# Kernel optimization log

Measured on AMD Instinct MI355X. Metric: run time of the kernel, lower is better.

The kernel has to match this reference:

```python
import jax, jax.numpy as jnp
import numpy as np

N_NODES = 50000
N_EDGES = 1250000
IN_CH, HID_CH, OUT_CH = 128, 64, 10
N_GRAPHS = 500


def gcn_conv(x, W, src, dst, n_nodes):
    # GCNConv (bias=False, normalize=True, add_self_loops=True):
    # out = D^{-1/2} (A + I) D^{-1/2} X W
    h = x @ W  # [N, H]
    loop = jnp.arange(n_nodes, dtype=src.dtype)
    s = jnp.concatenate([src, loop])
    d = jnp.concatenate([dst, loop])
    deg = jax.ops.segment_sum(jnp.ones_like(d, dtype=h.dtype), d, num_segments=n_nodes)
    dinv = jnp.where(deg > 0, jax.lax.rsqrt(deg), 0.0)
    norm = dinv[s] * dinv[d]  # [E+N]
    msgs = h[s] * norm[:, None]  # gather + normalize
    return jax.ops.segment_sum(msgs, d, num_segments=n_nodes)  # scatter-add


def setup_inputs() -> dict:
    key = jax.random.key(0)
    ks = jax.random.split(key, 8)
    x = jax.random.normal(ks[0], (N_NODES, IN_CH), dtype=jnp.float32)
    edge_index = jax.random.randint(ks[1], (2, N_EDGES), 0, N_NODES, dtype=jnp.int64)
    batch = jnp.sort(jax.random.randint(ks[2], (N_NODES,), 0, N_GRAPHS, dtype=jnp.int64))
    def glorot(k, fan_in, fan_out):
        lim = np.sqrt(6.0 / (fan_in + fan_out))
        return jax.random.uniform(k, (fan_in, fan_out), jnp.float32, -lim, lim)
    W1 = glorot(ks[3], IN_CH, HID_CH)
    W2 = glorot(ks[4], HID_CH, HID_CH)
    W3 = glorot(ks[5], HID_CH, HID_CH)
    Wl = glorot(ks[6], HID_CH, OUT_CH)
    bl = jnp.zeros((OUT_CH,), jnp.float32)
    return {"x": x, "edge_index": edge_index, "batch": batch,
            "W1": W1, "W2": W2, "W3": W3, "Wl": Wl, "bl": bl}


def reference(x, edge_index, batch, W1, W2, W3, Wl, bl):
    src, dst = edge_index[0], edge_index[1]
    n = x.shape[0]
    h = jax.nn.relu(gcn_conv(x, W1, src, dst, n))
    h = jax.nn.relu(gcn_conv(h, W2, src, dst, n))
    h = gcn_conv(h, W3, src, dst, n)
    # global_mean_pool over graph ids
    sums = jax.ops.segment_sum(h, batch, num_segments=N_GRAPHS)
    cnts = jax.ops.segment_sum(jnp.ones((n,), h.dtype), batch, num_segments=N_GRAPHS)
    pooled = sums / jnp.maximum(cnts, 1.0)[:, None]
    return pooled @ Wl + bl
```

## Files before the change

kernel.cpp:

```cpp
#include <hip/hip_runtime.h>

#define CH 64
#define CHUNK 4096
#define BSHIFT 8
#define NBUCK 196

__device__ __forceinline__ unsigned short f2bf_rne(float f) {
    unsigned int u = __float_as_uint(f);
    u += 0x7fffu + ((u >> 16) & 1u);
    return (unsigned short)(u >> 16);
}
__device__ __forceinline__ float bf_lo(unsigned int q) {
    return __uint_as_float(q << 16);
}
__device__ __forceinline__ float bf_hi(unsigned int q) {
    return __uint_as_float(q & 0xffff0000u);
}
__device__ __forceinline__ unsigned int pack2bf(float lo, float hi) {
    return (unsigned int)f2bf_rne(lo) | ((unsigned int)f2bf_rne(hi) << 16);
}

__global__ __launch_bounds__(256) void bucket_hist_kernel(
        const int* __restrict__ dst, int* __restrict__ bucket_cnt, int E) {
    __shared__ int hist[256];
    int tid = threadIdx.x;
    int e0 = blockIdx.x * CHUNK;
    int total = min(CHUNK, E - e0);
    hist[tid] = 0;
    __syncthreads();
    for (int i = tid; i < total; i += 256)
        atomicAdd(&hist[dst[e0 + i] >> BSHIFT], 1);
    __syncthreads();
    if (tid < NBUCK && hist[tid]) atomicAdd(&bucket_cnt[tid], hist[tid]);
}

__global__ __launch_bounds__(256) void bucket_scan_kernel(
        const int* __restrict__ cnt, int* __restrict__ base,
        int* __restrict__ cursor, int* __restrict__ rowptr, int N, int E) {
    __shared__ int sc[256];
    int tid = threadIdx.x;
    int c = (tid < NBUCK) ? cnt[tid] : 0;
    sc[tid] = c;
    __syncthreads();
    for (int off = 1; off < 256; off <<= 1) {
        int v = (tid >= off) ? sc[tid - off] : 0;
        __syncthreads();
        sc[tid] += v;
        __syncthreads();
    }
    if (tid < NBUCK) { base[tid] = sc[tid] - c; cursor[tid] = sc[tid] - c; }
    if (tid == NBUCK - 1) base[NBUCK] = sc[tid];
    if (tid == 0) rowptr[N] = E;
}

__global__ __launch_bounds__(256) void bin_kernel(
        const int* __restrict__ src, const int* __restrict__ dst,
        int* __restrict__ cursor, unsigned int* __restrict__ pairs, int E) {
    __shared__ unsigned int stage[CHUNK];
    __shared__ int hist[256], sc[256], lbase[256], lcur[256], gbase[256];
    int tid = threadIdx.x;
    int e0 = blockIdx.x * CHUNK;
    int total = min(CHUNK, E - e0);
    hist[tid] = 0;
    __syncthreads();
    for (int i = tid; i < total; i += 256)
        atomicAdd(&hist[dst[e0 + i] >> BSHIFT], 1);
    __syncthreads();
    sc[tid] = hist[tid];
    __syncthreads();
    for (int off = 1; off < 256; off <<= 1) {
        int v = (tid >= off) ? sc[tid - off] : 0;
        __syncthreads();
        sc[tid] += v;
        __syncthreads();
    }
    lbase[tid] = sc[tid] - hist[tid];
    lcur[tid]  = sc[tid] - hist[tid];
    if (tid < NBUCK && hist[tid] > 0) gbase[tid] = atomicAdd(&cursor[tid], hist[tid]);
    __syncthreads();
    for (int i = tid; i < total; i += 256) {
        unsigned int s = (unsigned int)src[e0 + i];
        unsigned int d = (unsigned int)dst[e0 + i];
        int pos = atomicAdd(&lcur[d >> BSHIFT], 1);
        stage[pos] = (d << 16) | s;
    }
    __syncthreads();
    for (int i = tid; i < total; i += 256) {
        unsigned int p = stage[i];
        int b = (int)(p >> 24);
        pairs[gbase[b] + (i - lbase[b])] = p;
    }
}

__global__ __launch_bounds__(256) void bucket_sort_kernel(
        const unsigned int* __restrict__ pairs, const int* __restrict__ base,
        int* __restrict__ csr, int* __restrict__ rowptr,
        float* __restrict__ dinv, int N) {
    __shared__ int cntl[256], sc[256], cur[256];
    int tid = threadIdx.x;
    int b = blockIdx.x;
    int pbase = base[b], pend = base[b + 1];
    int cnt = pend - pbase;
    cntl[tid] = 0;
    __syncthreads();
    for (int i = tid; i < cnt; i += 256)
        atomicAdd(&cntl[(pairs[pbase + i] >> 16) & 255u], 1);
    __syncthreads();
    sc[tid] = cntl[tid];
    __syncthreads();
    for (int off = 1; off < 256; off <<= 1) {
        int v = (tid >= off) ? sc[tid - off] : 0;
        __syncthreads();
        sc[tid] += v;
        __syncthreads();
    }
    int excl = sc[tid] - cntl[tid];
    cur[tid] = excl;
    int v = (b << BSHIFT) + tid;
    if (v < N) {
        rowptr[v] = pbase + excl;
        dinv[v] = rsqrtf((float)(cntl[tid] + 1));
    }
    __syncthreads();
    for (int i = tid; i < cnt; i += 256) {
        unsigned int p = pairs[pbase + i];
        int pos = atomicAdd(&cur[(p >> 16) & 255u], 1);
        csr[pbase + pos] = (int)(p & 0xffffu);
    }
}

template <int K>
__global__ __launch_bounds__(256) void gemm_f32_kernel(
        const float* __restrict__ X, const float* __restrict__ W,
        const float* __restrict__ dinv, unsigned short* __restrict__ G, int N) {
    constexpr int KC  = 64;
    constexpr int XLD = KC + 4;
    __shared__ float Xs[64 * XLD];
    __shared__ float Wls[KC * CH];
    int tid = threadIdx.x;
    int tx  = tid & 15;
    int ty  = tid >> 4;
    int row_tile = blockIdx.x * 64;
    int r0 = ty * 4;
    float acc[4][4] = {{0.f}};

    for (int kc = 0; kc < K; kc += KC) {
        __syncthreads();
#pragma unroll
        for (int t = 0; t < 4; ++t) {
            int idx = tid + t * 256;
            int row = idx >> 4;
            int k4  = idx & 15;
            int grow = row_tile + row;
            const float4* xs = (const float4*)(X + (size_t)min(grow, N - 1) * K + kc);
            *(float4*)&Xs[row * XLD + 4 * k4] = xs[k4];
        }
#pragma unroll
        for (int t = 0; t < 4; ++t) {
            int idx = tid + t * 256;
            *(float4*)&Wls[idx * 4] = ((const float4*)(W + (size_t)kc * CH))[idx];
        }
        __syncthreads();
#pragma unroll
        for (int kk = 0; kk < KC; kk += 4) {
            float xr[4][4], wr[4][4];
#pragma unroll
            for (int i = 0; i < 4; ++i) {
                float4 v = *(const float4*)&Xs[(r0 + i) * XLD + kk];
                xr[i][0] = v.x; xr[i][1] = v.y; xr[i][2] = v.z; xr[i][3] = v.w;
            }
#pragma unroll
            for (int j = 0; j < 4; ++j) {
                float4 v = *(const float4*)&Wls[(kk + j) * CH + 4 * tx];
                wr[j][0] = v.x; wr[j][1] = v.y; wr[j][2] = v.z; wr[j][3] = v.w;
            }
#pragma unroll
            for (int i = 0; i < 4; ++i)
#pragma unroll
                for (int j = 0; j < 4; ++j)
#pragma unroll
                    for (int c = 0; c < 4; ++c)
                        acc[i][c] = fmaf(xr[i][j], wr[j][c], acc[i][c]);
        }
    }
#pragma unroll
    for (int i = 0; i < 4; ++i) {
        int r = row_tile + r0 + i;
        if (r < N) {
            float d = dinv[r];
            ushort4 o;
            o.x = f2bf_rne(acc[i][0] * d);
            o.y = f2bf_rne(acc[i][1] * d);
            o.z = f2bf_rne(acc[i][2] * d);
            o.w = f2bf_rne(acc[i][3] * d);
            ((ushort4*)G)[(size_t)r * 16 + tx] = o;
        }
    }
}

__global__ __launch_bounds__(256) void gemm_bf16_kernel(
        const unsigned short* __restrict__ Xbf, const float* __restrict__ W,
        const float* __restrict__ dinv, unsigned short* __restrict__ G, int N) {
    constexpr int XLDU = 36;
    __shared__ unsigned int Xs[64 * XLDU];
    __shared__ float Wls[64 * CH];
    int tid = threadIdx.x;
    int tx  = tid & 15;
    int ty  = tid >> 4;
    int row_tile = blockIdx.x * 64;
    int r0 = ty * 4;
    float acc[4][4] = {{0.f}};

#pragma unroll
    for (int t = 0; t < 2; ++t) {
        int idx = tid + t * 256;
        int row = idx >> 3;
        int k4  = idx & 7;
        int grow = row_tile + row;
        uint4 v = ((const uint4*)Xbf)[(size_t)min(grow, N - 1) * 8 + k4];
        *(uint4*)&Xs[row * XLDU + 4 * k4] = v;
    }
#pragma unroll
    for (int t = 0; t < 4; ++t) {
        int idx = tid + t * 256;
        *(float4*)&Wls[idx * 4] = ((const float4*)W)[idx];
    }
    __syncthreads();
#pragma unroll
    for (int kk = 0; kk < 64; kk += 4) {
        float xr[4][4], wr[4][4];
#pragma unroll
        for (int i = 0; i < 4; ++i) {
            uint2 q = *(const uint2*)&Xs[(r0 + i) * XLDU + (kk >> 1)];
            xr[i][0] = bf_lo(q.x); xr[i][1] = bf_hi(q.x);
            xr[i][2] = bf_lo(q.y); xr[i][3] = bf_hi(q.y);
        }
#pragma unroll
        for (int j = 0; j < 4; ++j) {
            float4 v = *(const float4*)&Wls[(kk + j) * CH + 4 * tx];
            wr[j][0] = v.x; wr[j][1] = v.y; wr[j][2] = v.z; wr[j][3] = v.w;
        }
#pragma unroll
        for (int i = 0; i < 4; ++i)
#pragma unroll
            for (int j = 0; j < 4; ++j)
#pragma unroll
                for (int c = 0; c < 4; ++c)
                    acc[i][c] = fmaf(xr[i][j], wr[j][c], acc[i][c]);
    }
#pragma unroll
    for (int i = 0; i < 4; ++i) {
        int r = row_tile + r0 + i;
        if (r < N) {
            float d = dinv[r];
            ushort4 o;
            o.x = f2bf_rne(acc[i][0] * d);
            o.y = f2bf_rne(acc[i][1] * d);
            o.z = f2bf_rne(acc[i][2] * d);
            o.w = f2bf_rne(acc[i][3] * d);
            ((ushort4*)G)[(size_t)r * 16 + tx] = o;
        }
    }
}

template <bool F32OUT>
__global__ __launch_bounds__(256) void aggregate_kernel(
        const unsigned short* __restrict__ G, const int* __restrict__ rowptr,
        const int* __restrict__ csr, const float* __restrict__ dinv,
        void* __restrict__ Out, int N, int E, int relu) {
    int lane = threadIdx.x & 63;
    int w = (blockIdx.x * 256 + threadIdx.x) >> 6;
    int grp = lane >> 3;
    int cl  = lane & 7;
    int v = w * 8 + grp;
    bool valid = v < N;
    int vc = valid ? v : N - 1;
    int beg = rowptr[vc];
    int cnt = valid ? rowptr[vc + 1] - beg : 0;
    int mx = cnt;
    mx = max(mx, __shfl_xor(mx, 8));
    mx = max(mx, __shfl_xor(mx, 16));
    mx = max(mx, __shfl_xor(mx, 32));

    const uint4* __restrict__ G4 = (const uint4*)G;
    float a0 = 0.f, a1 = 0.f, a2 = 0.f, a3 = 0.f;
    float a4 = 0.f, a5 = 0.f, a6 = 0.f, a7 = 0.f;
#pragma unroll 2
    for (int it = 0; it < mx; ++it) {
        int eg = min(beg + it, E - 1);
        bool ok = it < cnt;
        int u = ok ? csr[eg] : 0;
        float s = ok ? 1.f : 0.f;
        uint4 q = G4[(size_t)u * 8 + cl];
        a0 = fmaf(bf_lo(q.x), s, a0); a1 = fmaf(bf_hi(q.x), s, a1);
        a2 = fmaf(bf_lo(q.y), s, a2); a3 = fmaf(bf_hi(q.y), s, a3);
        a4 = fmaf(bf_lo(q.z), s, a4); a5 = fmaf(bf_hi(q.z), s, a5);
        a6 = fmaf(bf_lo(q.w), s, a6); a7 = fmaf(bf_hi(q.w), s, a7);
    }
    if (valid) {
        uint4 q = G4[(size_t)v * 8 + cl];
        float d = dinv[v];
        float o0 = (a0 + bf_lo(q.x)) * d, o1 = (a1 + bf_hi(q.x)) * d;
        float o2 = (a2 + bf_lo(q.y)) * d, o3 = (a3 + bf_hi(q.y)) * d;
        float o4 = (a4 + bf_lo(q.z)) * d, o5 = (a5 + bf_hi(q.z)) * d;
        float o6 = (a6 + bf_lo(q.w)) * d, o7 = (a7 + bf_hi(q.w)) * d;
        if (relu) {
            o0 = fmaxf(o0, 0.f); o1 = fmaxf(o1, 0.f); o2 = fmaxf(o2, 0.f);
            o3 = fmaxf(o3, 0.f); o4 = fmaxf(o4, 0.f); o5 = fmaxf(o5, 0.f);
            o6 = fmaxf(o6, 0.f); o7 = fmaxf(o7, 0.f);
        }
        if (F32OUT) {
            float4 w0 = {o0, o1, o2, o3}, w1 = {o4, o5, o6, o7};
            ((float4*)Out)[(size_t)v * 16 + cl * 2]     = w0;
            ((float4*)Out)[(size_t)v * 16 + cl * 2 + 1] = w1;
        } else {
            uint4 p;
            p.x = pack2bf(o0, o1); p.y = pack2bf(o2, o3);
            p.z = pack2bf(o4, o5); p.w = pack2bf(o6, o7);
            ((uint4*)Out)[(size_t)v * 8 + cl] = p;
        }
    }
}

__global__ void gptr_kernel(const int* __restrict__ batch, int* __restrict__ gptr,
                            int N, int NG) {
    int g = blockIdx.x * blockDim.x + threadIdx.x;
    if (g > NG) return;
    if (g == NG) { gptr[NG] = N; return; }
    int lo = 0, hi = N;
    while (lo < hi) {
        int mid = (lo + hi) >> 1;
        if (batch[mid] < g) lo = mid + 1; else hi = mid;
    }
    gptr[g] = lo;
}

__global__ __launch_bounds__(64) void pool_head_kernel(
        const float* __restrict__ H, const int* __restrict__ gptr,
        const float* __restrict__ Wl, const float* __restrict__ bl,
        float* __restrict__ out, int NG) {
    int g = blockIdx.x;
    int lane = threadIdx.x;
    int s = gptr[g], e = gptr[g + 1];
    float acc = 0.f;
    for (int v = s; v < e; ++v) acc += H[(size_t)v * CH + lane];
    float c = (float)(e - s);
    float mean = (c > 0.f) ? acc / c : 0.f;
    for (int o = 0; o < 10; ++o) {
        float t = mean * Wl[lane * 10 + o];
        for (int off = 32; off > 0; off >>= 1) t += __shfl_down(t, off);
        if (lane == 0) out[g * 10 + o] = t + bl[o];
    }
}

extern "C" void kernel_launch(void* const* d_in, const int* in_sizes, int n_in,
                              void* d_out, int out_size, void* d_ws, size_t ws_size,
                              hipStream_t stream) {
    const float* x     = (const float*)d_in[0];
    const int*   ei    = (const int*)d_in[1];
    const int*   batch = (const int*)d_in[2];
    const float* W1    = (const float*)d_in[3];
    const float* W2    = (const float*)d_in[4];
    const float* W3    = (const float*)d_in[5];
    const float* Wl    = (const float*)d_in[6];
    const float* bl    = (const float*)d_in[7];
    float* out = (float*)d_out;

    const int N  = in_sizes[0] / 128;
    const int E  = in_sizes[1] / 2;
    const int NG = out_size / 10;

    const int* src = ei;
    const int* dst = ei + E;

    char* ws = (char*)d_ws;
    size_t off = 0;
    auto alloc = [&](size_t bytes) -> void* {
        void* p = ws + off;
        off += bytes;
        off = (off + 255) & ~(size_t)255;
        return p;
    };
    int*   bucket_cnt    = (int*)alloc((size_t)NBUCK * 4);
    int*   bucket_base   = (int*)alloc((size_t)(NBUCK + 1) * 4);
    int*   bucket_cursor = (int*)alloc((size_t)NBUCK * 4);
    int*   csr    = (int*)alloc((size_t)(E + 64) * 4);
    int*   rowptr = (int*)alloc((size_t)(N + 1) * 4);
    float* dinv   = (float*)alloc((size_t)N * 4);
    int*   gptr   = (int*)alloc((size_t)(NG + 1) * 4);
    unsigned short* Gbf = (unsigned short*)alloc((size_t)N * CH * 2);
    unsigned short* Hbf = (unsigned short*)alloc((size_t)N * CH * 2);
    float* hbuf   = (float*)alloc((size_t)N * CH * 4);
    unsigned int* pairs = (unsigned int*)hbuf;

    hipMemsetAsync(bucket_cnt, 0, (size_t)NBUCK * 4, stream);

    int cb = (E + CHUNK - 1) / CHUNK;
    int ab = ((N + 7) / 8 + 3) / 4;
    int gb = (N + 63) / 64;

    bucket_hist_kernel<<<cb, 256, 0, stream>>>(dst, bucket_cnt, E);
    bucket_scan_kernel<<<1, 256, 0, stream>>>(bucket_cnt, bucket_base, bucket_cursor,
                                              rowptr, N, E);
    bin_kernel<<<cb, 256, 0, stream>>>(src, dst, bucket_cursor, pairs, E);
    bucket_sort_kernel<<<NBUCK, 256, 0, stream>>>(pairs, bucket_base, csr, rowptr, dinv, N);
    gptr_kernel<<<(NG + 512) / 512, 512, 0, stream>>>(batch, gptr, N, NG);

    gemm_f32_kernel<128><<<gb, 256, 0, stream>>>(x, W1, dinv, Gbf, N);
    aggregate_kernel<false><<<ab, 256, 0, stream>>>(Gbf, rowptr, csr, dinv, Hbf, N, E, 1);
    gemm_bf16_kernel<<<gb, 256, 0, stream>>>(Hbf, W2, dinv, Gbf, N);
    aggregate_kernel<false><<<ab, 256, 0, stream>>>(Gbf, rowptr, csr, dinv, Hbf, N, E, 1);
    gemm_bf16_kernel<<<gb, 256, 0, stream>>>(Hbf, W3, dinv, Gbf, N);
    aggregate_kernel<true><<<ab, 256, 0, stream>>>(Gbf, rowptr, csr, dinv, hbuf, N, E, 0);

    pool_head_kernel<<<NG, 64, 0, stream>>>(hbuf, gptr, Wl, bl, out, NG);
}
```

Measured before the change: 251.2 us.

## Fuse first GEMM with edge histogram, use per-chunk offsets and 16-bit CSR

Runs the first GEMM and the per-chunk destination histogram as one launch, so the GEMM no longer waits for dinv. The first aggregation therefore applies the source dinv per edge. A single scan kernel computes deterministic per-chunk bucket offsets, replacing the memset, the global atomic cursor and the separate scan. Graph pointers are computed inside that same scan kernel, and CSR column indices are stored as 16-bit values to halve index traffic. The costs are an extra per-edge dinv gather in layer one and a serial loop over chunks in a single scan block.

```diff
diff --git a/kernel.cpp b/kernel.cpp
--- a/kernel.cpp
+++ b/kernel.cpp
@@ -20,42 +20,138 @@
     return (unsigned int)f2bf_rne(lo) | ((unsigned int)f2bf_rne(hi) << 16);
 }
 
-__global__ __launch_bounds__(256) void bucket_hist_kernel(
-        const int* __restrict__ dst, int* __restrict__ bucket_cnt, int E) {
+template <int K>
+__global__ __launch_bounds__(256) void gemm1_hist_kernel(
+        const float* __restrict__ X, const float* __restrict__ W,
+        unsigned short* __restrict__ G, int N,
+        const int* __restrict__ dst, int* __restrict__ chunk_hist, int E,
+        int gemm_blocks) {
+    constexpr int KC  = 64;
+    constexpr int XLD = KC + 4;
+    __shared__ float Xs[64 * XLD];
+    __shared__ float Wls[KC * CH];
     __shared__ int hist[256];
     int tid = threadIdx.x;
-    int e0 = blockIdx.x * CHUNK;
-    int total = min(CHUNK, E - e0);
-    hist[tid] = 0;
-    __syncthreads();
-    for (int i = tid; i < total; i += 256)
-        atomicAdd(&hist[dst[e0 + i] >> BSHIFT], 1);
-    __syncthreads();
-    if (tid < NBUCK && hist[tid]) atomicAdd(&bucket_cnt[tid], hist[tid]);
-}
-
-__global__ __launch_bounds__(256) void bucket_scan_kernel(
-        const int* __restrict__ cnt, int* __restrict__ base,
-        int* __restrict__ cursor, int* __restrict__ rowptr, int N, int E) {
-    __shared__ int sc[256];
-    int tid = threadIdx.x;
-    int c = (tid < NBUCK) ? cnt[tid] : 0;
-    sc[tid] = c;
-    __syncthreads();
-    for (int off = 1; off < 256; off <<= 1) {
-        int v = (tid >= off) ? sc[tid - off] : 0;
-        __syncthreads();
-        sc[tid] += v;
-        __syncthreads();
-    }
-    if (tid < NBUCK) { base[tid] = sc[tid] - c; cursor[tid] = sc[tid] - c; }
-    if (tid == NBUCK - 1) base[NBUCK] = sc[tid];
-    if (tid == 0) rowptr[N] = E;
+
+    if (blockIdx.x >= gemm_blocks) {
+        int cid = blockIdx.x - gemm_blocks;
+        int e0 = cid * CHUNK;
+        int total = min(CHUNK, E - e0);
+        hist[tid] = 0;
+        __syncthreads();
+        for (int i = tid; i < total; i += 256)
+            atomicAdd(&hist[dst[e0 + i] >> BSHIFT], 1);
+        __syncthreads();
+        if (tid < NBUCK) chunk_hist[cid * NBUCK + tid] = hist[tid];
+        return;
+    }
+
+    int tx  = tid & 15;
+    int ty  = tid >> 4;
+    int row_tile = blockIdx.x * 64;
+    int r0 = ty * 4;
+    float acc[4][4] = {{0.f}};
+
+    for (int kc = 0; kc < K; kc += KC) {
+        __syncthreads();
+#pragma unroll
+        for (int t = 0; t < 4; ++t) {
+            int idx = tid + t * 256;
+            int row = idx >> 4;
+            int k4  = idx & 15;
+            int grow = row_tile + row;
+            const float4* xs = (const float4*)(X + (size_t)min(grow, N - 1) * K + kc);
+            *(float4*)&Xs[row * XLD + 4 * k4] = xs[k4];
+        }
+#pragma unroll
+        for (int t = 0; t < 4; ++t) {
+            int idx = tid + t * 256;
+            *(float4*)&Wls[idx * 4] = ((const float4*)(W + (size_t)kc * CH))[idx];
+        }
+        __syncthreads();
+#pragma unroll
+        for (int kk = 0; kk < KC; kk += 4) {
+            float xr[4][4], wr[4][4];
+#pragma unroll
+            for (int i = 0; i < 4; ++i) {
+                float4 v = *(const float4*)&Xs[(r0 + i) * XLD + kk];
+                xr[i][0] = v.x; xr[i][1] = v.y; xr[i][2] = v.z; xr[i][3] = v.w;
+            }
+#pragma unroll
+            for (int j = 0; j < 4; ++j) {
+                float4 v = *(const float4*)&Wls[(kk + j) * CH + 4 * tx];
+                wr[j][0] = v.x; wr[j][1] = v.y; wr[j][2] = v.z; wr[j][3] = v.w;
+            }
+#pragma unroll
+            for (int i = 0; i < 4; ++i)
+#pragma unroll
+                for (int j = 0; j < 4; ++j)
+#pragma unroll
+                    for (int c = 0; c < 4; ++c)
+                        acc[i][c] = fmaf(xr[i][j], wr[j][c], acc[i][c]);
+        }
+    }
+#pragma unroll
+    for (int i = 0; i < 4; ++i) {
+        int r = row_tile + r0 + i;
+        if (r < N) {
+            ushort4 o;
+            o.x = f2bf_rne(acc[i][0]);
+            o.y = f2bf_rne(acc[i][1]);
+            o.z = f2bf_rne(acc[i][2]);
+            o.w = f2bf_rne(acc[i][3]);
+            ((ushort4*)G)[(size_t)r * 16 + tx] = o;
+        }
+    }
+}
+
+__global__ __launch_bounds__(256) void scan_gptr_kernel(
+        const int* __restrict__ chunk_hist, int cb,
+        int* __restrict__ chunk_base, int* __restrict__ bucket_base,
+        int* __restrict__ rowptr,
+        const int* __restrict__ batch, int* __restrict__ gptr,
+        int N, int E, int NG) {
+    if (blockIdx.x == 0) {
+        __shared__ int sc[256];
+        int t = threadIdx.x;
+        int total = 0;
+        if (t < NBUCK)
+            for (int c = 0; c < cb; ++c) total += chunk_hist[c * NBUCK + t];
+        sc[t] = total;
+        __syncthreads();
+        for (int off = 1; off < 256; off <<= 1) {
+            int v = (t >= off) ? sc[t - off] : 0;
+            __syncthreads();
+            sc[t] += v;
+            __syncthreads();
+        }
+        int base = sc[t] - total;
+        if (t < NBUCK) {
+            bucket_base[t] = base;
+            int run = base;
+            for (int c = 0; c < cb; ++c) {
+                chunk_base[c * NBUCK + t] = run;
+                run += chunk_hist[c * NBUCK + t];
+            }
+        }
+        if (t == NBUCK - 1) bucket_base[NBUCK] = sc[t];
+        if (t == 0) rowptr[N] = E;
+    } else {
+        for (int g = threadIdx.x; g <= NG; g += 256) {
+            if (g == NG) { gptr[NG] = N; continue; }
+            int lo = 0, hi = N;
+            while (lo < hi) {
+                int mid = (lo + hi) >> 1;
+                if (batch[mid] < g) lo = mid + 1; else hi = mid;
+            }
+            gptr[g] = lo;
+        }
+    }
 }
 
 __global__ __launch_bounds__(256) void bin_kernel(
         const int* __restrict__ src, const int* __restrict__ dst,
-        int* __restrict__ cursor, unsigned int* __restrict__ pairs, int E) {
+        const int* __restrict__ chunk_base, unsigned int* __restrict__ pairs, int E) {
     __shared__ unsigned int stage[CHUNK];
     __shared__ int hist[256], sc[256], lbase[256], lcur[256], gbase[256];
     int tid = threadIdx.x;
@@ -76,7 +172,7 @@
     }
     lbase[tid] = sc[tid] - hist[tid];
     lcur[tid]  = sc[tid] - hist[tid];
-    if (tid < NBUCK && hist[tid] > 0) gbase[tid] = atomicAdd(&cursor[tid], hist[tid]);
+    if (tid < NBUCK) gbase[tid] = chunk_base[blockIdx.x * NBUCK + tid];
     __syncthreads();
     for (int i = tid; i < total; i += 256) {
         unsigned int s = (unsigned int)src[e0 + i];
@@ -94,7 +190,7 @@
 
 __global__ __launch_bounds__(256) void bucket_sort_kernel(
         const unsigned int* __restrict__ pairs, const int* __restrict__ base,
-        int* __restrict__ csr, int* __restrict__ rowptr,
+        unsigned short* __restrict__ csr, int* __restrict__ rowptr,
         float* __restrict__ dinv, int N) {
     __shared__ int cntl[256], sc[256], cur[256];
     int tid = threadIdx.x;
@@ -125,75 +221,67 @@
     for (int i = tid; i < cnt; i += 256) {
         unsigned int p = pairs[pbase + i];
         int pos = atomicAdd(&cur[(p >> 16) & 255u], 1);
-        csr[pbase + pos] = (int)(p & 0xffffu);
-    }
-}
-
-template <int K>
-__global__ __launch_bounds__(256) void gemm_f32_kernel(
-        const float* __restrict__ X, const float* __restrict__ W,
-        const float* __restrict__ dinv, unsigned short* __restrict__ G, int N) {
-    constexpr int KC  = 64;
-    constexpr int XLD = KC + 4;
-    __shared__ float Xs[64 * XLD];
-    __shared__ float Wls[KC * CH];
-    int tid = threadIdx.x;
-    int tx  = tid & 15;
-    int ty  = tid >> 4;
-    int row_tile = blockIdx.x * 64;
-    int r0 = ty * 4;
-    float acc[4][4] = {{0.f}};
-
-    for (int kc = 0; kc < K; kc += KC) {
-        __syncthreads();
-#pragma unroll
-        for (int t = 0; t < 4; ++t) {
-            int idx = tid + t * 256;
-            int row = idx >> 4;
-            int k4  = idx & 15;
-            int grow = row_tile + row;
-            const float4* xs = (const float4*)(X + (size_t)min(grow, N - 1) * K + kc);
-            *(float4*)&Xs[row * XLD + 4 * k4] = xs[k4];
-        }
-#pragma unroll
-        for (int t = 0; t < 4; ++t) {
-            int idx = tid + t * 256;
-            *(float4*)&Wls[idx * 4] = ((const float4*)(W + (size_t)kc * CH))[idx];
-        }
-        __syncthreads();
-#pragma unroll
-        for (int kk = 0; kk < KC; kk += 4) {
-            float xr[4][4], wr[4][4];
-#pragma unroll
-            for (int i = 0; i < 4; ++i) {
-                float4 v = *(const float4*)&Xs[(r0 + i) * XLD + kk];
-                xr[i][0] = v.x; xr[i][1] = v.y; xr[i][2] = v.z; xr[i][3] = v.w;
-            }
-#pragma unroll
-            for (int j = 0; j < 4; ++j) {
-                float4 v = *(const float4*)&Wls[(kk + j) * CH + 4 * tx];
-                wr[j][0] = v.x; wr[j][1] = v.y; wr[j][2] = v.z; wr[j][3] = v.w;
-            }
-#pragma unroll
-            for (int i = 0; i < 4; ++i)
-#pragma unroll
-                for (int j = 0; j < 4; ++j)
-#pragma unroll
-                    for (int c = 0; c < 4; ++c)
-                        acc[i][c] = fmaf(xr[i][j], wr[j][c], acc[i][c]);
-        }
-    }
-#pragma unroll
-    for (int i = 0; i < 4; ++i) {
-        int r = row_tile + r0 + i;
-        if (r < N) {
-            float d = dinv[r];
-            ushort4 o;
-            o.x = f2bf_rne(acc[i][0] * d);
-            o.y = f2bf_rne(acc[i][1] * d);
-            o.z = f2bf_rne(acc[i][2] * d);
-            o.w = f2bf_rne(acc[i][3] * d);
-            ((ushort4*)G)[(size_t)r * 16 + tx] = o;
+        csr[pbase + pos] = (unsigned short)(p & 0xffffu);
+    }
+}
+
+template <bool PRESCALED, bool F32OUT>
+__global__ __launch_bounds__(256) void aggregate_kernel(
+        const unsigned short* __restrict__ G, const int* __restrict__ rowptr,
+        const unsigned short* __restrict__ csr, const float* __restrict__ dinv,
+        void* __restrict__ Out, int N, int E, int relu) {
+    int lane = threadIdx.x & 63;
+    int w = (blockIdx.x * 256 + threadIdx.x) >> 6;
+    int grp = lane >> 3, cl = lane & 7;
+    int v = w * 8 + grp;
+    bool valid = v < N;
+    int vc = valid ? v : N - 1;
+    int beg = rowptr[vc];
+    int cnt = valid ? rowptr[vc + 1] - beg : 0;
+    int mx = cnt;
+    mx = max(mx, __shfl_xor(mx, 8));
+    mx = max(mx, __shfl_xor(mx, 16));
+    mx = max(mx, __shfl_xor(mx, 32));
+
+    const uint4* __restrict__ G4 = (const uint4*)G;
+    float a0 = 0.f, a1 = 0.f, a2 = 0.f, a3 = 0.f;
+    float a4 = 0.f, a5 = 0.f, a6 = 0.f, a7 = 0.f;
+#pragma unroll 2
+    for (int it = 0; it < mx; ++it) {
+        int eg = min(beg + it, E - 1);
+        bool ok = it < cnt;
+        int u = ok ? (int)csr[eg] : 0;
+        float s;
+        if (PRESCALED) s = ok ? 1.f : 0.f;
+        else           s = ok ? dinv[u] : 0.f;
+        uint4 q = G4[(size_t)u * 8 + cl];
+        a0 = fmaf(bf_lo(q.x), s, a0); a1 = fmaf(bf_hi(q.x), s, a1);
+        a2 = fmaf(bf_lo(q.y), s, a2); a3 = fmaf(bf_hi(q.y), s, a3);
+        a4 = fmaf(bf_lo(q.z), s, a4); a5 = fmaf(bf_hi(q.z), s, a5);
+        a6 = fmaf(bf_lo(q.w), s, a6); a7 = fmaf(bf_hi(q.w), s, a7);
+    }
+    if (valid) {
+        uint4 q = G4[(size_t)v * 8 + cl];
+        float d = dinv[v];
+        float sv = PRESCALED ? 1.f : d;
+        float o0 = (a0 + bf_lo(q.x) * sv) * d, o1 = (a1 + bf_hi(q.x) * sv) * d;
+        float o2 = (a2 + bf_lo(q.y) * sv) * d, o3 = (a3 + bf_hi(q.y) * sv) * d;
+        float o4 = (a4 + bf_lo(q.z) * sv) * d, o5 = (a5 + bf_hi(q.z) * sv) * d;
+        float o6 = (a6 + bf_lo(q.w) * sv) * d, o7 = (a7 + bf_hi(q.w) * sv) * d;
+        if (relu) {
+            o0 = fmaxf(o0, 0.f); o1 = fmaxf(o1, 0.f); o2 = fmaxf(o2, 0.f);
+            o3 = fmaxf(o3, 0.f); o4 = fmaxf(o4, 0.f); o5 = fmaxf(o5, 0.f);
+            o6 = fmaxf(o6, 0.f); o7 = fmaxf(o7, 0.f);
+        }
+        if (F32OUT) {
+            float4 w0 = {o0, o1, o2, o3}, w1 = {o4, o5, o6, o7};
+            ((float4*)Out)[(size_t)v * 16 + cl * 2]     = w0;
+            ((float4*)Out)[(size_t)v * 16 + cl * 2 + 1] = w1;
+        } else {
+            uint4 p;
+            p.x = pack2bf(o0, o1); p.y = pack2bf(o2, o3);
+            p.z = pack2bf(o4, o5); p.w = pack2bf(o6, o7);
+            ((uint4*)Out)[(size_t)v * 8 + cl] = p;
         }
     }
 }
@@ -261,78 +349,6 @@
             ((ushort4*)G)[(size_t)r * 16 + tx] = o;
         }
     }
-}
-
-template <bool F32OUT>
-__global__ __launch_bounds__(256) void aggregate_kernel(
-        const unsigned short* __restrict__ G, const int* __restrict__ rowptr,
-        const int* __restrict__ csr, const float* __restrict__ dinv,
-        void* __restrict__ Out, int N, int E, int relu) {
-    int lane = threadIdx.x & 63;
-    int w = (blockIdx.x * 256 + threadIdx.x) >> 6;
-    int grp = lane >> 3;
-    int cl  = lane & 7;
-    int v = w * 8 + grp;
-    bool valid = v < N;
-    int vc = valid ? v : N - 1;
-    int beg = rowptr[vc];
-    int cnt = valid ? rowptr[vc + 1] - beg : 0;
-    int mx = cnt;
-    mx = max(mx, __shfl_xor(mx, 8));
-    mx = max(mx, __shfl_xor(mx, 16));
-    mx = max(mx, __shfl_xor(mx, 32));
-
-    const uint4* __restrict__ G4 = (const uint4*)G;
-    float a0 = 0.f, a1 = 0.f, a2 = 0.f, a3 = 0.f;
-    float a4 = 0.f, a5 = 0.f, a6 = 0.f, a7 = 0.f;
-#pragma unroll 2
-    for (int it = 0; it < mx; ++it) {
-        int eg = min(beg + it, E - 1);
-        bool ok = it < cnt;
-        int u = ok ? csr[eg] : 0;
-        float s = ok ? 1.f : 0.f;
-        uint4 q = G4[(size_t)u * 8 + cl];
-        a0 = fmaf(bf_lo(q.x), s, a0); a1 = fmaf(bf_hi(q.x), s, a1);
-        a2 = fmaf(bf_lo(q.y), s, a2); a3 = fmaf(bf_hi(q.y), s, a3);
-        a4 = fmaf(bf_lo(q.z), s, a4); a5 = fmaf(bf_hi(q.z), s, a5);
-        a6 = fmaf(bf_lo(q.w), s, a6); a7 = fmaf(bf_hi(q.w), s, a7);
-    }
-    if (valid) {
-        uint4 q = G4[(size_t)v * 8 + cl];
-        float d = dinv[v];
-        float o0 = (a0 + bf_lo(q.x)) * d, o1 = (a1 + bf_hi(q.x)) * d;
-        float o2 = (a2 + bf_lo(q.y)) * d, o3 = (a3 + bf_hi(q.y)) * d;
-        float o4 = (a4 + bf_lo(q.z)) * d, o5 = (a5 + bf_hi(q.z)) * d;
-        float o6 = (a6 + bf_lo(q.w)) * d, o7 = (a7 + bf_hi(q.w)) * d;
-        if (relu) {
-            o0 = fmaxf(o0, 0.f); o1 = fmaxf(o1, 0.f); o2 = fmaxf(o2, 0.f);
-            o3 = fmaxf(o3, 0.f); o4 = fmaxf(o4, 0.f); o5 = fmaxf(o5, 0.f);
-            o6 = fmaxf(o6, 0.f); o7 = fmaxf(o7, 0.f);
-        }
-        if (F32OUT) {
-            float4 w0 = {o0, o1, o2, o3}, w1 = {o4, o5, o6, o7};
-            ((float4*)Out)[(size_t)v * 16 + cl * 2]     = w0;
-            ((float4*)Out)[(size_t)v * 16 + cl * 2 + 1] = w1;
-        } else {
-            uint4 p;
-            p.x = pack2bf(o0, o1); p.y = pack2bf(o2, o3);
-            p.z = pack2bf(o4, o5); p.w = pack2bf(o6, o7);
-            ((uint4*)Out)[(size_t)v * 8 + cl] = p;
-        }
-    }
-}
-
-__global__ void gptr_kernel(const int* __restrict__ batch, int* __restrict__ gptr,
-                            int N, int NG) {
-    int g = blockIdx.x * blockDim.x + threadIdx.x;
-    if (g > NG) return;
-    if (g == NG) { gptr[NG] = N; return; }
-    int lo = 0, hi = N;
-    while (lo < hi) {
-        int mid = (lo + hi) >> 1;
-        if (batch[mid] < g) lo = mid + 1; else hi = mid;
-    }
-    gptr[g] = lo;
 }
 
 __global__ __launch_bounds__(64) void pool_head_kernel(
@@ -373,6 +389,8 @@
     const int* src = ei;
     const int* dst = ei + E;
 
+    const int cb = (E + CHUNK - 1) / CHUNK;
+
     char* ws = (char*)d_ws;
     size_t off = 0;
     auto alloc = [&](size_t bytes) -> void* {
@@ -381,37 +399,36 @@
         off = (off + 255) & ~(size_t)255;
         return p;
     };
-    int*   bucket_cnt    = (int*)alloc((size_t)NBUCK * 4);
-    int*   bucket_base   = (int*)alloc((size_t)(NBUCK + 1) * 4);
-    int*   bucket_cursor = (int*)alloc((size_t)NBUCK * 4);
-    int*   csr    = (int*)alloc((size_t)(E + 64) * 4);
+    int*   chunk_hist  = (int*)alloc((size_t)cb * NBUCK * 4);
+    int*   chunk_base  = (int*)alloc((size_t)cb * NBUCK * 4);
+    int*   bucket_base = (int*)alloc((size_t)(NBUCK + 1) * 4);
+    unsigned short* csr = (unsigned short*)alloc((size_t)(E + 64) * 2);
     int*   rowptr = (int*)alloc((size_t)(N + 1) * 4);
     float* dinv   = (float*)alloc((size_t)N * 4);
-    int*   gptr   = (int*)alloc((size_t)(NG + 1) * 4);
-    unsigned short* Gbf = (unsigned short*)alloc((size_t)N * CH * 2);
-    unsigned short* Hbf = (unsigned short*)alloc((size_t)N * CH * 2);
+    int*   gptrb  = (int*)alloc((size_t)(NG + 1) * 4);
+    unsigned short* GA = (unsigned short*)alloc((size_t)N * CH * 2);
+    unsigned short* GB = (unsigned short*)alloc((size_t)N * CH * 2);
     float* hbuf   = (float*)alloc((size_t)N * CH * 4);
     unsigned int* pairs = (unsigned int*)hbuf;
 
-    hipMemsetAsync(bucket_cnt, 0, (size_t)NBUCK * 4, stream);
-
-    int cb = (E + CHUNK - 1) / CHUNK;
+    int gb = (N + 63) / 64;
     int ab = ((N + 7) / 8 + 3) / 4;
-    int gb = (N + 63) / 64;
-
-    bucket_hist_kernel<<<cb, 256, 0, stream>>>(dst, bucket_cnt, E);
-    bucket_scan_kernel<<<1, 256, 0, stream>>>(bucket_cnt, bucket_base, bucket_cursor,
-                                              rowptr, N, E);
-    bin_kernel<<<cb, 256, 0, stream>>>(src, dst, bucket_cursor, pairs, E);
+
+    gemm1_hist_kernel<128><<<gb + cb, 256, 0, stream>>>(x, W1, GA, N,
+                                                        dst, chunk_hist, E, gb);
+    scan_gptr_kernel<<<2, 256, 0, stream>>>(chunk_hist, cb, chunk_base, bucket_base,
+                                            rowptr, batch, gptrb, N, E, NG);
+    bin_kernel<<<cb, 256, 0, stream>>>(src, dst, chunk_base, pairs, E);
     bucket_sort_kernel<<<NBUCK, 256, 0, stream>>>(pairs, bucket_base, csr, rowptr, dinv, N);
-    gptr_kernel<<<(NG + 512) / 512, 512, 0, stream>>>(batch, gptr, N, NG);
-
-    gemm_f32_kernel<128><<<gb, 256, 0, stream>>>(x, W1, dinv, Gbf, N);
-    aggregate_kernel<false><<<ab, 256, 0, stream>>>(Gbf, rowptr, csr, dinv, Hbf, N, E, 1);
-    gemm_bf16_kernel<<<gb, 256, 0, stream>>>(Hbf, W2, dinv, Gbf, N);
-    aggregate_kernel<false><<<ab, 256, 0, stream>>>(Gbf, rowptr, csr, dinv, Hbf, N, E, 1);
-    gemm_bf16_kernel<<<gb, 256, 0, stream>>>(Hbf, W3, dinv, Gbf, N);
-    aggregate_kernel<true><<<ab, 256, 0, stream>>>(Gbf, rowptr, csr, dinv, hbuf, N, E, 0);
-
-    pool_head_kernel<<<NG, 64, 0, stream>>>(hbuf, gptr, Wl, bl, out, NG);
-}
+
+    aggregate_kernel<false, false><<<ab, 256, 0, stream>>>(GA, rowptr, csr, dinv,
+                                                           GB, N, E, 1);
+    gemm_bf16_kernel<<<gb, 256, 0, stream>>>(GB, W2, dinv, GA, N);
+    aggregate_kernel<true, false><<<ab, 256, 0, stream>>>(GA, rowptr, csr, dinv,
+                                                          GB, N, E, 1);
+    gemm_bf16_kernel<<<gb, 256, 0, stream>>>(GB, W3, dinv, GA, N);
+    aggregate_kernel<true, true><<<ab, 256, 0, stream>>>(GA, rowptr, csr, dinv,
+                                                         hbuf, N, E, 0);
+
+    pool_head_kernel<<<NG, 64, 0, stream>>>(hbuf, gptrb, Wl, bl, out, NG);
+}
```

Result: slower. 297.8 us (+18.5%).
